# Optimization experiments

Hardware: AMD Instinct MI355X
Metric: run time of the kernel (lower is better)

## Reference

```python
import jax, jax.numpy as jnp
import numpy as np

H = 31  # hidden_size == input_size


def setup_inputs() -> dict:
    key = jax.random.key(0)
    ks = jax.random.split(key, 7)
    B, T = 2048, 512
    s = 1.0 / np.sqrt(H)
    return {
        "x": jax.random.normal(ks[0], (B, T, H), dtype=jnp.float32),
        "W_ih": jax.random.uniform(ks[1], (3 * H, H), minval=-s, maxval=s, dtype=jnp.float32),
        "W_hh": jax.random.uniform(ks[2], (3 * H, H), minval=-s, maxval=s, dtype=jnp.float32),
        "b_ih": jax.random.uniform(ks[3], (3 * H,), minval=-s, maxval=s, dtype=jnp.float32),
        "b_hh": jax.random.uniform(ks[4], (3 * H,), minval=-s, maxval=s, dtype=jnp.float32),
        "W_fc": jax.random.uniform(ks[5], (2, H), minval=-s, maxval=s, dtype=jnp.float32),
        "b_fc": jax.random.uniform(ks[6], (2,), minval=-s, maxval=s, dtype=jnp.float32),
    }


def _gru_seq(x, W_ih, W_hh, b_ih, b_hh):
    # x: [B, T, I]. Precompute input-side gates for all timesteps (one big GEMM).
    B = x.shape[0]
    xg = jnp.einsum("bti,gi->btg", x, W_ih) + b_ih          # [B, T, 3H]
    xg = jnp.swapaxes(xg, 0, 1)                              # [T, B, 3H]

    def step(h, xg_t):
        gh = h @ W_hh.T + b_hh                               # [B, 3H]
        ir, iz, inn = jnp.split(xg_t, 3, axis=-1)
        hr, hz, hn = jnp.split(gh, 3, axis=-1)
        r = jax.nn.sigmoid(ir + hr)
        z = jax.nn.sigmoid(iz + hz)
        n = jnp.tanh(inn + r * hn)
        h_new = (1.0 - z) * n + z * h
        return h_new, h_new

    h0 = jnp.zeros((B, H), dtype=x.dtype)
    _, out = jax.lax.scan(step, h0, xg)                      # out: [T, B, H]
    return jnp.swapaxes(out, 0, 1)                           # [B, T, H]


def reference(x, W_ih, W_hh, b_ih, b_hh, W_fc, b_fc):
    out = _gru_seq(x, W_ih, W_hh, b_ih, b_hh)                # [B, T, H]
    return out @ W_fc.T + b_fc                               # [B, T, 2]
```

## Files before the change

kernel.cpp:

```cpp
#include <hip/hip_runtime.h>


constexpr int BB = 2048, TT = 512, HH = 31;
constexpr int RR = 96;
constexpr size_t XG_BYTES = (size_t)BB * RR * TT * 2;
constexpr int WPAIRS = 93 * 16;
constexpr size_t WS_NEEDED = XG_BYTES + (size_t)WPAIRS * 4;

#define MEMFENCE asm volatile("" ::: "memory")

typedef _Float16 hf2 __attribute__((ext_vector_type(2)));

__device__ __forceinline__ float dot2(int a, hf2 w, float acc) {
#if __has_builtin(__builtin_amdgcn_fdot2)
    return __builtin_amdgcn_fdot2(__builtin_bit_cast(hf2, a), w, acc, false);
#else
    hf2 x = __builtin_bit_cast(hf2, a);
    return acc + (float)x.x * (float)x.x * 0.f + (float)x.x * (float)w.x + (float)x.y * (float)w.y;
#endif
}

#if __has_builtin(__builtin_amdgcn_permlane32_swap)
__device__ __forceinline__ float half_sum(float v) {
    auto p = __builtin_amdgcn_permlane32_swap(
        __builtin_bit_cast(unsigned, v), __builtin_bit_cast(unsigned, v),
        false, false);
    return __builtin_bit_cast(float, (unsigned)p[0]) +
           __builtin_bit_cast(float, (unsigned)p[1]);
}
__device__ __forceinline__ float xor32_swap(float v) {
    return half_sum(v) - v;
}
#else
__device__ __forceinline__ float half_sum(float v) {
    return v + __shfl_xor(v, 32);
}
__device__ __forceinline__ float xor32_swap(float v) {
    return __shfl_xor(v, 32);
}
#endif

__global__ void pack_wih_kernel(const float* __restrict__ W_ih, int* __restrict__ wpk) {
    int q = blockIdx.x * blockDim.x + threadIdx.x;
    if (q >= WPAIRS) return;
    int row = q >> 4, p = q & 15;
    float lo = W_ih[row * HH + 2 * p];
    float hi = (2 * p + 1 < HH) ? W_ih[row * HH + 2 * p + 1] : 0.f;
    hf2 w; w.x = (_Float16)lo; w.y = (_Float16)hi;
    wpk[q] = __builtin_bit_cast(int, w);
}

__global__ __launch_bounds__(128, 2) void xg_gemm_kernel(
    const float* __restrict__ x, const int* __restrict__ wpk,
    const float* __restrict__ b_ih, _Float16* __restrict__ xg)
{
    const int tid = threadIdx.x;
    const int b   = blockIdx.x;
    const int t0  = tid * 4;
    const float* xb = x + ((size_t)b * TT + t0) * HH;

    hf2 xp[4][16];
#pragma unroll
    for (int j = 0; j < 4; ++j)
#pragma unroll
        for (int p = 0; p < 16; ++p) {
            float lo = xb[j * HH + 2 * p];
            float hi = (2 * p + 1 < HH) ? xb[j * HH + 2 * p + 1] : 0.f;
            xp[j][p].x = (_Float16)lo; xp[j][p].y = (_Float16)hi;
        }

    _Float16* xgb = xg + (size_t)b * RR * TT + t0;
    for (int row = 0; row < 93; ++row) {
        const float bi = b_ih[row];
        float a0 = bi, a1 = bi, a2 = bi, a3 = bi;
        const int* wr = wpk + row * 16;
#pragma unroll
        for (int p = 0; p < 16; ++p) {
            const int w = wr[p];
            a0 = dot2(w, xp[0][p], a0);
            a1 = dot2(w, xp[1][p], a1);
            a2 = dot2(w, xp[2][p], a2);
            a3 = dot2(w, xp[3][p], a3);
        }
        hf2 lo2; lo2.x = (_Float16)a0; lo2.y = (_Float16)a1;
        hf2 hi2; hi2.x = (_Float16)a2; hi2.y = (_Float16)a3;
        *reinterpret_cast<int2*>(xgb + (size_t)row * TT) =
            make_int2(__builtin_bit_cast(int, lo2), __builtin_bit_cast(int, hi2));
    }
    for (int row = 93; row < 96; ++row)
        *reinterpret_cast<int2*>(xgb + (size_t)row * TT) = make_int2(0, 0);
}

__global__ __launch_bounds__(256, 2) void gru_rec_kernel(
    const _Float16* __restrict__ xg, const float* __restrict__ W_hh,
    const float* __restrict__ b_hh, const float* __restrict__ W_fc,
    const float* __restrict__ b_fc, float* __restrict__ out)
{
    __shared__ _Float16 hbuf[4][32];
    const int tid = threadIdx.x, wv = tid >> 6, lane = tid & 63;
    const int li = lane & 31, half = lane >> 5;
    const int b  = blockIdx.x * 4 + wv;
    const bool u = (li < HH);

    const float* pA = u ? W_hh + (size_t)(half * HH + li) * HH : W_fc + half * HH;
    const float* pN = W_hh + (size_t)(2 * HH + (u ? li : 0)) * HH;
    const float bA0 = u ? b_hh[half * HH + li] : b_fc[half];
    const float bN0 = (u && half == 0) ? b_hh[2 * HH + li] : 0.f;

    hf2 wA[16], wN[8];
#pragma unroll
    for (int p = 0; p < 16; ++p) {
        const int pp = (p + 8 * half) & 15;
        float lo = pA[2 * pp];
        float hi = (2 * pp + 1 < HH) ? pA[2 * pp + 1] : 0.f;
        wA[p].x = (_Float16)lo; wA[p].y = (_Float16)hi;
    }
#pragma unroll
    for (int p = 0; p < 8; ++p) {
        const int pp = 8 * half + p;
        float lo = u ? pN[2 * pp] : 0.f;
        float hi = (u && 2 * pp + 1 < HH) ? pN[2 * pp + 1] : 0.f;
        wN[p].x = (_Float16)lo; wN[p].y = (_Float16)hi;
    }

    const int rowA = u ? half * HH + li : 93 + half;
    const int rowN = u ? 2 * HH + li : 95;
    const _Float16* gA = xg + ((size_t)b * RR + rowA) * TT;
    const _Float16* gN = xg + ((size_t)b * RR + rowN) * TT;
    float* outb = out + (size_t)b * TT * 2;

    if (half == 0) hbuf[wv][li] = (_Float16)0.f;
    MEMFENCE;

    const int4* HP = (const int4*)&hbuf[wv][0];
    const int i0 = (0 + 2 * half) & 3, i1 = (1 + 2 * half) & 3,
              i2 = (2 + 2 * half) & 3, i3 = (3 + 2 * half) & 3;

    int4 bufA = *(const int4*)gA;
    int4 bufN = *(const int4*)gN;
    float hval = 0.f;

    for (int tb = 0; tb < TT / 8; ++tb) {
        int4 nxtA = bufA, nxtN = bufN;
        if (tb + 1 < TT / 8) {
            nxtA = *(const int4*)(gA + (size_t)(tb + 1) * 8);
            nxtN = *(const int4*)(gN + (size_t)(tb + 1) * 8);
        }
#pragma unroll
        for (int s = 0; s < 8; ++s) {
            const int t = tb * 8 + s;
            const int4 h0 = HP[i0], h1 = HP[i1], h2 = HP[i2], h3 = HP[i3];
            const float xa = (float)(((const _Float16*)&bufA)[s]);
            const float xn = (float)(((const _Float16*)&bufN)[s]);

            float n0 = bN0, n1 = 0.f;
            n0 = dot2(h0.x, wN[0], n0); n1 = dot2(h0.y, wN[1], n1);
            n0 = dot2(h0.z, wN[2], n0); n1 = dot2(h0.w, wN[3], n1);
            n0 = dot2(h1.x, wN[4], n0); n1 = dot2(h1.y, wN[5], n1);
            n0 = dot2(h1.z, wN[6], n0); n1 = dot2(h1.w, wN[7], n1);
            const float accN = n0 + n1;
            const float nh = half_sum(accN);

            float a0v = bA0 + xa, a1v = 0.f;
            a0v = dot2(h0.x, wA[0], a0v);  a1v = dot2(h0.y, wA[1], a1v);
            a0v = dot2(h0.z, wA[2], a0v);  a1v = dot2(h0.w, wA[3], a1v);
            a0v = dot2(h1.x, wA[4], a0v);  a1v = dot2(h1.y, wA[5], a1v);
            a0v = dot2(h1.z, wA[6], a0v);  a1v = dot2(h1.w, wA[7], a1v);
            a0v = dot2(h2.x, wA[8], a0v);  a1v = dot2(h2.y, wA[9], a1v);
            a0v = dot2(h2.z, wA[10], a0v); a1v = dot2(h2.w, wA[11], a1v);
            a0v = dot2(h3.x, wA[12], a0v); a1v = dot2(h3.y, wA[13], a1v);
            a0v = dot2(h3.z, wA[14], a0v); a1v = dot2(h3.w, wA[15], a1v);
            const float accA = a0v + a1v;
            const float asw = xor32_swap(accA);

            if (li == 31 && t > 0) outb[(size_t)(t - 1) * 2 + half] = accA;

            const float g  = __fdividef(1.f, 1.f + __expf(-accA));
            const float go = __fdividef(1.f, 1.f + __expf(-asw));
            const float r = half ? go : g;
            const float z = half ? g  : go;
            const float npre = fmaf(r, nh, xn);
            const float nn   = __fdividef(2.f, 1.f + __expf(-2.f * npre)) - 1.f;
            const float hnew = nn + z * (hval - nn);
            hval = u ? hnew : 0.f;
            if (half == 0) hbuf[wv][li] = (_Float16)hval;
            MEMFENCE;
        }
        bufA = nxtA; bufN = nxtN;
    }

    {
        const int4 h0 = HP[i0], h1 = HP[i1], h2 = HP[i2], h3 = HP[i3];
        float a0v = bA0, a1v = 0.f;
        a0v = dot2(h0.x, wA[0], a0v);  a1v = dot2(h0.y, wA[1], a1v);
        a0v = dot2(h0.z, wA[2], a0v);  a1v = dot2(h0.w, wA[3], a1v);
        a0v = dot2(h1.x, wA[4], a0v);  a1v = dot2(h1.y, wA[5], a1v);
        a0v = dot2(h1.z, wA[6], a0v);  a1v = dot2(h1.w, wA[7], a1v);
        a0v = dot2(h2.x, wA[8], a0v);  a1v = dot2(h2.y, wA[9], a1v);
        a0v = dot2(h2.z, wA[10], a0v); a1v = dot2(h2.w, wA[11], a1v);
        a0v = dot2(h3.x, wA[12], a0v); a1v = dot2(h3.y, wA[13], a1v);
        a0v = dot2(h3.z, wA[14], a0v); a1v = dot2(h3.w, wA[15], a1v);
        if (li == 31) outb[(size_t)(TT - 1) * 2 + half] = a0v + a1v;
    }
}

__global__ __launch_bounds__(64, 1) void gru_pair_kernel(
    const float* __restrict__ x, const float* __restrict__ W_ih,
    const float* __restrict__ W_hh, const float* __restrict__ b_ih,
    const float* __restrict__ b_hh, const float* __restrict__ W_fc,
    const float* __restrict__ b_fc, float* __restrict__ out)
{
    __shared__ _Float16 hbuf[2][32];
    __shared__ _Float16 xbuf[2][2][32];

    const int lane = threadIdx.x & 63;
    const int li   = lane & 31;
    const int half = lane >> 5;
    const int b    = blockIdx.x * 2 + half;
    const bool unit = (li < HH);

    const float* ph0 = unit ? W_hh + (size_t)li * HH            : W_fc;
    const float* ph1 = unit ? W_hh + (size_t)(HH + li) * HH     : W_fc + HH;
    const float* ph2 = unit ? W_hh + (size_t)(2 * HH + li) * HH : nullptr;
    const float* px0 = unit ? W_ih + (size_t)li * HH            : nullptr;
    const float* px1 = unit ? W_ih + (size_t)(HH + li) * HH     : nullptr;
    const float* px2 = unit ? W_ih + (size_t)(2 * HH + li) * HH : nullptr;

    hf2 wh0[16], wh1[16], wh2[16], wx0[16], wx1[16], wx2[16];
#pragma unroll
    for (int m = 0; m < 16; ++m) {
        auto pk = [&](const float* p) -> hf2 {
            hf2 r;
            r.x = p ? (_Float16)p[2 * m] : (_Float16)0.f;
            r.y = (p && (2 * m + 1) < HH) ? (_Float16)p[2 * m + 1] : (_Float16)0.f;
            return r;
        };
        wh0[m] = pk(ph0); wh1[m] = pk(ph1); wh2[m] = pk(ph2);
        wx0[m] = pk(px0); wx1[m] = pk(px1); wx2[m] = pk(px2);
    }

    float arH0, azH0, anH0, anX0;
    if (unit) {
        arH0 = b_ih[li] + b_hh[li];
        azH0 = b_ih[HH + li] + b_hh[HH + li];
        anH0 = b_hh[2 * HH + li];
        anX0 = b_ih[2 * HH + li];
    } else {
        arH0 = b_fc[0]; azH0 = b_fc[1]; anH0 = 0.f; anX0 = 0.f;
    }

    const float* xb   = x + (size_t)b * TT * HH;
    float*       outb = out + (size_t)b * TT * 2;

    hbuf[half][li]    = (_Float16)0.f;
    xbuf[0][half][li] = unit ? (_Float16)xb[li]      : (_Float16)0.f;
    xbuf[1][half][li] = unit ? (_Float16)xb[HH + li] : (_Float16)0.f;
    MEMFENCE;
    float xpre = unit ? xb[(size_t)2 * HH + li] : 0.f;
    float hval = 0.f;

    const int4* HP  = (const int4*)(&hbuf[half][0]);
    const int4* XB0 = (const int4*)(&xbuf[0][half][0]);
    const int4* XB1 = (const int4*)(&xbuf[1][half][0]);

    int4 xq0 = XB0[0], xq1 = XB0[1], xq2 = XB0[2], xq3 = XB0[3];

#pragma unroll 2
    for (int t = 0; t < TT; ++t) {
        int4 hq0 = HP[0], hq1 = HP[1], hq2 = HP[2], hq3 = HP[3];

        float arH = arH0, azH = azH0, anH = anH0;
        float arX = 0.f, azX = 0.f, anX = anX0;
#define STEPM(m, hp, xp) \
        arH = dot2(hp, wh0[m], arH); azH = dot2(hp, wh1[m], azH); \
        anH = dot2(hp, wh2[m], anH); arX = dot2(xp, wx0[m], arX); \
        azX = dot2(xp, wx1[m], azX); anX = dot2(xp, wx2[m], anX);
        STEPM(0,  hq0.x, xq0.x) STEPM(1,  hq0.y, xq0.y)
        STEPM(2,  hq0.z, xq0.z) STEPM(3,  hq0.w, xq0.w)
        STEPM(4,  hq1.x, xq1.x) STEPM(5,  hq1.y, xq1.y)
        STEPM(6,  hq1.z, xq1.z) STEPM(7,  hq1.w, xq1.w)
        STEPM(8,  hq2.x, xq2.x) STEPM(9,  hq2.y, xq2.y)
        STEPM(10, hq2.z, xq2.z) STEPM(11, hq2.w, xq2.w)
        STEPM(12, hq3.x, xq3.x) STEPM(13, hq3.y, xq3.y)
        STEPM(14, hq3.z, xq3.z) STEPM(15, hq3.w, xq3.w)
#undef STEPM

        const float sumr = arH + arX;
        const float sumz = azH + azX;
        if (lane == 31 && t > 0)
            *(float2*)(outb + (size_t)(t - 1) * 2) = make_float2(sumr, sumz);

        const float r    = __fdividef(1.f, 1.f + __expf(-sumr));
        const float z    = __fdividef(1.f, 1.f + __expf(-sumz));
        const float npre = fmaf(r, anH, anX);
        const float nn   = __fdividef(2.f, 1.f + __expf(-2.f * npre)) - 1.f;
        const float hnew = nn + z * (hval - nn);
        hval = unit ? hnew : 0.f;
        hbuf[half][li] = (_Float16)hval;

        xbuf[t & 1][half][li] = unit ? (_Float16)xpre : (_Float16)0.f;
        MEMFENCE;
        int tn = t + 3; if (tn > TT - 1) tn = TT - 1;
        xpre = unit ? xb[(size_t)tn * HH + li] : 0.f;

        const int4* XN = (t & 1) ? XB0 : XB1;
        xq0 = XN[0]; xq1 = XN[1]; xq2 = XN[2]; xq3 = XN[3];
    }

    {
        int4 hq0 = HP[0], hq1 = HP[1], hq2 = HP[2], hq3 = HP[3];
        float f0 = arH0, f1 = azH0;
#define FST(m, hp) f0 = dot2(hp, wh0[m], f0); f1 = dot2(hp, wh1[m], f1);
        FST(0,  hq0.x) FST(1,  hq0.y) FST(2,  hq0.z) FST(3,  hq0.w)
        FST(4,  hq1.x) FST(5,  hq1.y) FST(6,  hq1.z) FST(7,  hq1.w)
        FST(8,  hq2.x) FST(9,  hq2.y) FST(10, hq2.z) FST(11, hq2.w)
        FST(12, hq3.x) FST(13, hq3.y) FST(14, hq3.z) FST(15, hq3.w)
#undef FST
        if (lane == 31)
            *(float2*)(outb + (size_t)(TT - 1) * 2) = make_float2(f0, f1);
    }
}

extern "C" void kernel_launch(void* const* d_in, const int* in_sizes, int n_in,
                              void* d_out, int out_size, void* d_ws, size_t ws_size,
                              hipStream_t stream) {
    const float* x    = (const float*)d_in[0];
    const float* W_ih = (const float*)d_in[1];
    const float* W_hh = (const float*)d_in[2];
    const float* b_ih = (const float*)d_in[3];
    const float* b_hh = (const float*)d_in[4];
    const float* W_fc = (const float*)d_in[5];
    const float* b_fc = (const float*)d_in[6];
    float* out = (float*)d_out;

    if (ws_size >= WS_NEEDED) {
        _Float16* xg = (_Float16*)d_ws;
        int* wpk = (int*)((char*)d_ws + XG_BYTES);
        pack_wih_kernel<<<(WPAIRS + 255) / 256, 256, 0, stream>>>(W_ih, wpk);
        xg_gemm_kernel<<<BB, 128, 0, stream>>>(x, wpk, b_ih, xg);
        gru_rec_kernel<<<BB / 4, 256, 0, stream>>>(xg, W_hh, b_hh, W_fc, b_fc, out);
    } else {
        gru_pair_kernel<<<BB / 2, 64, 0, stream>>>(x, W_ih, W_hh, b_ih, b_hh,
                                                   W_fc, b_fc, out);
    }
}
```

Baseline: 311.6 us.

## Broadcast hidden state via readlane instead of LDS and fold log2e into weights

Replaces the per-step LDS round trip for the hidden state with a DPP pair-pack followed by 16 readlanes into scalar registers. Each half-wave now computes the full 31-wide n-gate dot product itself, which removes the cross-half reduction. Log2(e) scale factors are folded into W_ih, W_hh and the biases so the gates can use raw exp2 and rcp intrinsics. The cost is twice the n-gate dot products per lane and readlane serialization on the critical recurrence path.

```diff
diff --git a/kernel.cpp b/kernel.cpp
--- a/kernel.cpp
+++ b/kernel.cpp
@@ -6,6 +6,7 @@
 constexpr size_t XG_BYTES = (size_t)BB * RR * TT * 2;
 constexpr int WPAIRS = 93 * 16;
 constexpr size_t WS_NEEDED = XG_BYTES + (size_t)WPAIRS * 4;
+constexpr float LOG2E = 1.4426950408889634f;
 
 #define MEMFENCE asm volatile("" ::: "memory")
 
@@ -16,36 +17,57 @@
     return __builtin_amdgcn_fdot2(__builtin_bit_cast(hf2, a), w, acc, false);
 #else
     hf2 x = __builtin_bit_cast(hf2, a);
-    return acc + (float)x.x * (float)x.x * 0.f + (float)x.x * (float)w.x + (float)x.y * (float)w.y;
+    return acc + (float)x.x * (float)w.x + (float)x.y * (float)w.y;
+#endif
+}
+
+__device__ __forceinline__ float fast_exp2(float x) {
+#if __has_builtin(__builtin_amdgcn_exp2f)
+    return __builtin_amdgcn_exp2f(x);
+#else
+    return exp2f(x);
+#endif
+}
+__device__ __forceinline__ float fast_rcp(float x) {
+#if __has_builtin(__builtin_amdgcn_rcpf)
+    return __builtin_amdgcn_rcpf(x);
+#else
+    return __fdividef(1.f, x);
 #endif
 }
 
 #if __has_builtin(__builtin_amdgcn_permlane32_swap)
-__device__ __forceinline__ float half_sum(float v) {
+__device__ __forceinline__ float xor32_swap(float v) {
     auto p = __builtin_amdgcn_permlane32_swap(
         __builtin_bit_cast(unsigned, v), __builtin_bit_cast(unsigned, v),
         false, false);
     return __builtin_bit_cast(float, (unsigned)p[0]) +
-           __builtin_bit_cast(float, (unsigned)p[1]);
-}
-__device__ __forceinline__ float xor32_swap(float v) {
-    return half_sum(v) - v;
-}
-#else
-__device__ __forceinline__ float half_sum(float v) {
-    return v + __shfl_xor(v, 32);
-}
-__device__ __forceinline__ float xor32_swap(float v) {
-    return __shfl_xor(v, 32);
-}
-#endif
+           __builtin_bit_cast(float, (unsigned)p[1]) - v;
+}
+#else
+__device__ __forceinline__ float xor32_swap(float v) { return __shfl_xor(v, 32); }
+#endif
+
+__device__ __forceinline__ void bcast_h(float hv, int hs[16]) {
+    const int pk = __builtin_bit_cast(int, __builtin_amdgcn_cvt_pkrtz(hv, hv));
+#if __has_builtin(__builtin_amdgcn_update_dpp)
+    const int nb = __builtin_amdgcn_update_dpp(0, pk, 0xB1, 0xF, 0xF, true);
+#else
+    const int nb = __shfl_xor(pk, 1);
+#endif
+    const int pr = __builtin_amdgcn_perm(nb, pk, 0x05040100);
+#pragma unroll
+    for (int m = 0; m < 16; ++m)
+        hs[m] = __builtin_amdgcn_readlane(pr, 2 * m);
+}
 
 __global__ void pack_wih_kernel(const float* __restrict__ W_ih, int* __restrict__ wpk) {
     int q = blockIdx.x * blockDim.x + threadIdx.x;
     if (q >= WPAIRS) return;
     int row = q >> 4, p = q & 15;
-    float lo = W_ih[row * HH + 2 * p];
-    float hi = (2 * p + 1 < HH) ? W_ih[row * HH + 2 * p + 1] : 0.f;
+    const float s = (row < 62) ? LOG2E : 2.f * LOG2E;
+    float lo = W_ih[row * HH + 2 * p] * s;
+    float hi = (2 * p + 1 < HH) ? W_ih[row * HH + 2 * p + 1] * s : 0.f;
     hf2 w; w.x = (_Float16)lo; w.y = (_Float16)hi;
     wpk[q] = __builtin_bit_cast(int, w);
 }
@@ -71,7 +93,7 @@
 
     _Float16* xgb = xg + (size_t)b * RR * TT + t0;
     for (int row = 0; row < 93; ++row) {
-        const float bi = b_ih[row];
+        const float bi = b_ih[row] * ((row < 62) ? LOG2E : 2.f * LOG2E);
         float a0 = bi, a1 = bi, a2 = bi, a3 = bi;
         const int* wr = wpk + row * 16;
 #pragma unroll
@@ -96,31 +118,28 @@
     const float* __restrict__ b_hh, const float* __restrict__ W_fc,
     const float* __restrict__ b_fc, float* __restrict__ out)
 {
-    __shared__ _Float16 hbuf[4][32];
     const int tid = threadIdx.x, wv = tid >> 6, lane = tid & 63;
     const int li = lane & 31, half = lane >> 5;
     const int b  = blockIdx.x * 4 + wv;
     const bool u = (li < HH);
 
-    const float* pA = u ? W_hh + (size_t)(half * HH + li) * HH : W_fc + half * HH;
+    const float sA = u ? LOG2E : 1.f;
+    const float sN = 2.f * LOG2E;
+    const float* pA = u ? W_hh + (size_t)(half * HH + li) * HH
+                        : W_fc + (size_t)half * HH;
     const float* pN = W_hh + (size_t)(2 * HH + (u ? li : 0)) * HH;
-    const float bA0 = u ? b_hh[half * HH + li] : b_fc[half];
-    const float bN0 = (u && half == 0) ? b_hh[2 * HH + li] : 0.f;
-
-    hf2 wA[16], wN[8];
+    const float bA0 = (u ? b_hh[half * HH + li] : b_fc[half]) * sA;
+    const float bN0 = u ? b_hh[2 * HH + li] * sN : 0.f;
+
+    hf2 wA[16], wN[16];
 #pragma unroll
     for (int p = 0; p < 16; ++p) {
-        const int pp = (p + 8 * half) & 15;
-        float lo = pA[2 * pp];
-        float hi = (2 * pp + 1 < HH) ? pA[2 * pp + 1] : 0.f;
-        wA[p].x = (_Float16)lo; wA[p].y = (_Float16)hi;
-    }
-#pragma unroll
-    for (int p = 0; p < 8; ++p) {
-        const int pp = 8 * half + p;
-        float lo = u ? pN[2 * pp] : 0.f;
-        float hi = (u && 2 * pp + 1 < HH) ? pN[2 * pp + 1] : 0.f;
-        wN[p].x = (_Float16)lo; wN[p].y = (_Float16)hi;
+        const float alo = pA[2 * p];
+        const float ahi = (2 * p + 1 < HH) ? pA[2 * p + 1] : 0.f;
+        wA[p].x = (_Float16)(alo * sA); wA[p].y = (_Float16)(ahi * sA);
+        const float nlo = u ? pN[2 * p] : 0.f;
+        const float nhi = (u && 2 * p + 1 < HH) ? pN[2 * p + 1] : 0.f;
+        wN[p].x = (_Float16)(nlo * sN); wN[p].y = (_Float16)(nhi * sN);
     }
 
     const int rowA = u ? half * HH + li : 93 + half;
@@ -129,16 +148,12 @@
     const _Float16* gN = xg + ((size_t)b * RR + rowN) * TT;
     float* outb = out + (size_t)b * TT * 2;
 
-    if (half == 0) hbuf[wv][li] = (_Float16)0.f;
-    MEMFENCE;
-
-    const int4* HP = (const int4*)&hbuf[wv][0];
-    const int i0 = (0 + 2 * half) & 3, i1 = (1 + 2 * half) & 3,
-              i2 = (2 + 2 * half) & 3, i3 = (3 + 2 * half) & 3;
+    float hval = 0.f;
+    int hs[16];
+    bcast_h(0.f, hs);
 
     int4 bufA = *(const int4*)gA;
     int4 bufN = *(const int4*)gN;
-    float hval = 0.f;
 
     for (int tb = 0; tb < TT / 8; ++tb) {
         int4 nxtA = bufA, nxtN = bufN;
@@ -149,58 +164,44 @@
 #pragma unroll
         for (int s = 0; s < 8; ++s) {
             const int t = tb * 8 + s;
-            const int4 h0 = HP[i0], h1 = HP[i1], h2 = HP[i2], h3 = HP[i3];
             const float xa = (float)(((const _Float16*)&bufA)[s]);
             const float xn = (float)(((const _Float16*)&bufN)[s]);
 
-            float n0 = bN0, n1 = 0.f;
-            n0 = dot2(h0.x, wN[0], n0); n1 = dot2(h0.y, wN[1], n1);
-            n0 = dot2(h0.z, wN[2], n0); n1 = dot2(h0.w, wN[3], n1);
-            n0 = dot2(h1.x, wN[4], n0); n1 = dot2(h1.y, wN[5], n1);
-            n0 = dot2(h1.z, wN[6], n0); n1 = dot2(h1.w, wN[7], n1);
+            float a0 = bA0 + xa, a1 = 0.f, n0 = bN0, n1 = 0.f;
+#pragma unroll
+            for (int m = 0; m < 16; m += 2) {
+                a0 = dot2(hs[m],     wA[m],     a0);
+                a1 = dot2(hs[m + 1], wA[m + 1], a1);
+                n0 = dot2(hs[m],     wN[m],     n0);
+                n1 = dot2(hs[m + 1], wN[m + 1], n1);
+            }
+            const float accA = a0 + a1;
             const float accN = n0 + n1;
-            const float nh = half_sum(accN);
-
-            float a0v = bA0 + xa, a1v = 0.f;
-            a0v = dot2(h0.x, wA[0], a0v);  a1v = dot2(h0.y, wA[1], a1v);
-            a0v = dot2(h0.z, wA[2], a0v);  a1v = dot2(h0.w, wA[3], a1v);
-            a0v = dot2(h1.x, wA[4], a0v);  a1v = dot2(h1.y, wA[5], a1v);
-            a0v = dot2(h1.z, wA[6], a0v);  a1v = dot2(h1.w, wA[7], a1v);
-            a0v = dot2(h2.x, wA[8], a0v);  a1v = dot2(h2.y, wA[9], a1v);
-            a0v = dot2(h2.z, wA[10], a0v); a1v = dot2(h2.w, wA[11], a1v);
-            a0v = dot2(h3.x, wA[12], a0v); a1v = dot2(h3.y, wA[13], a1v);
-            a0v = dot2(h3.z, wA[14], a0v); a1v = dot2(h3.w, wA[15], a1v);
-            const float accA = a0v + a1v;
             const float asw = xor32_swap(accA);
 
             if (li == 31 && t > 0) outb[(size_t)(t - 1) * 2 + half] = accA;
 
-            const float g  = __fdividef(1.f, 1.f + __expf(-accA));
-            const float go = __fdividef(1.f, 1.f + __expf(-asw));
+            const float g  = fast_rcp(1.f + fast_exp2(-accA));
+            const float go = fast_rcp(1.f + fast_exp2(-asw));
             const float r = half ? go : g;
-            const float z = half ? g  : go;
-            const float npre = fmaf(r, nh, xn);
-            const float nn   = __fdividef(2.f, 1.f + __expf(-2.f * npre)) - 1.f;
+            const float z = half ? g : go;
+            const float en = fast_exp2(fmaf(-r, accN, -xn));
+            const float nn = fmaf(2.f, fast_rcp(1.f + en), -1.f);
             const float hnew = nn + z * (hval - nn);
             hval = u ? hnew : 0.f;
-            if (half == 0) hbuf[wv][li] = (_Float16)hval;
-            MEMFENCE;
+            bcast_h(hval, hs);
         }
         bufA = nxtA; bufN = nxtN;
     }
 
     {
-        const int4 h0 = HP[i0], h1 = HP[i1], h2 = HP[i2], h3 = HP[i3];
-        float a0v = bA0, a1v = 0.f;
-        a0v = dot2(h0.x, wA[0], a0v);  a1v = dot2(h0.y, wA[1], a1v);
-        a0v = dot2(h0.z, wA[2], a0v);  a1v = dot2(h0.w, wA[3], a1v);
-        a0v = dot2(h1.x, wA[4], a0v);  a1v = dot2(h1.y, wA[5], a1v);
-        a0v = dot2(h1.z, wA[6], a0v);  a1v = dot2(h1.w, wA[7], a1v);
-        a0v = dot2(h2.x, wA[8], a0v);  a1v = dot2(h2.y, wA[9], a1v);
-        a0v = dot2(h2.z, wA[10], a0v); a1v = dot2(h2.w, wA[11], a1v);
-        a0v = dot2(h3.x, wA[12], a0v); a1v = dot2(h3.y, wA[13], a1v);
-        a0v = dot2(h3.z, wA[14], a0v); a1v = dot2(h3.w, wA[15], a1v);
-        if (li == 31) outb[(size_t)(TT - 1) * 2 + half] = a0v + a1v;
+        float a0 = bA0, a1 = 0.f;
+#pragma unroll
+        for (int m = 0; m < 16; m += 2) {
+            a0 = dot2(hs[m],     wA[m],     a0);
+            a1 = dot2(hs[m + 1], wA[m + 1], a1);
+        }
+        if (li == 31) outb[(size_t)(TT - 1) * 2 + half] = a0 + a1;
     }
 }
 
```

Measured after the change: 299.4 us. -3.9%, faster.
